# Kernel tuning notes

Hardware: AMD Instinct MI355X
Metric: run time of the kernel (lower is better)

The kernel has to match this reference:

```python
import jax, jax.numpy as jnp
import numpy as np

B, H, HKV, S, D = 1, 32, 4, 2048, 128
NEG = -1e9  # causal mask fill (float32-safe, like torch finfo.min in spirit)


def setup_inputs() -> dict:
    key = jax.random.key(0)
    kq, kk, kv, ks = jax.random.split(key, 4)
    query = jax.random.normal(kq, (B, H, S, D), dtype=jnp.float32)
    k = jax.random.normal(kk, (B, HKV, S, D), dtype=jnp.float32)
    v = jax.random.normal(kv, (B, HKV, S, D), dtype=jnp.float32)
    sinks = jax.random.normal(ks, (H,), dtype=jnp.float32)
    # causal additive mask [B, 1, S, S]
    causal = jnp.where(jnp.tril(jnp.ones((S, S), dtype=bool)), 0.0, NEG).astype(jnp.float32)
    attention_mask = jnp.broadcast_to(causal[None, None], (B, 1, S, S))
    return {"query": query, "key": k, "value": v,
            "attention_mask": attention_mask, "sinks": sinks}


def reference(query, key, value, attention_mask, sinks):
    scaling = 1.0 / jnp.sqrt(jnp.asarray(D, dtype=query.dtype))
    groups = H // HKV
    # repeat_kv: [B, HKV, S, D] -> [B, H, S, D]
    k = jnp.repeat(key, groups, axis=1)
    v = jnp.repeat(value, groups, axis=1)
    # scores [B, H, S, S]
    attn = jnp.einsum('bhqd,bhkd->bhqk', query, k) * scaling
    attn = attn + attention_mask[:, :, :, :attn.shape[-1]]
    # append per-head sink column -> [B, H, S, S+1]
    sink_col = jnp.broadcast_to(sinks.reshape(1, H, 1, 1), (B, H, S, 1)).astype(attn.dtype)
    combined = jnp.concatenate([attn, sink_col], axis=-1)
    combined = combined - jnp.max(combined, axis=-1, keepdims=True)
    probs = jax.nn.softmax(combined, axis=-1)[..., :-1]
    # PV matmul, then [B, H, S, D] -> [B, S, H, D]
    out = jnp.einsum('bhqk,bhkd->bhqd', probs, v)
    return jnp.transpose(out, (0, 2, 1, 3))
```

## Files before the change

kernel.cpp:

```cpp
#include <hip/hip_runtime.h>
#include <hip/hip_bf16.h>

#define NH   32
#define SEQ  2048
#define HD   128
#define KVB  32
#define TILE_ELEMS (KVB * HD)
#define TILE_BYTES 8192

typedef __attribute__((ext_vector_type(8))) short bf16x8;
typedef __attribute__((ext_vector_type(4))) float f32x4;
typedef __attribute__((ext_vector_type(2))) unsigned int u32x2;

#define VMCNT0 asm volatile("s_waitcnt vmcnt(0)" ::: "memory")

static __device__ __forceinline__ unsigned short f2bf(float f) {
  __hip_bfloat16 h = __float2bfloat16(f);
  union { __hip_bfloat16 h; unsigned short u; } c; c.h = h;
  return c.u;
}

__device__ __forceinline__ int swzK(int row, int colByte) {
  return row * 256 + (colByte ^ ((row & 7) << 4));
}
__device__ __forceinline__ int swzV32(int d, int kvByte) {
  return d * 64 + (kvByte ^ ((d & 3) << 4));
}
__device__ __forceinline__ int swzP32(int row, int colByte) {
  return row * 64 + (colByte ^ ((row & 3) << 4));
}

__global__ __launch_bounds__(256)
void convert_kv(const float* __restrict__ K, const float* __restrict__ V,
                char* __restrict__ Ki, char* __restrict__ Vi)
{
  const int b = blockIdx.x;
  const float* Ks = K + (size_t)b * TILE_ELEMS;
  const float* Vs = V + (size_t)b * TILE_ELEMS;
  char* kt = Ki + (size_t)b * TILE_BYTES;
  char* vt = Vi + (size_t)b * TILE_BYTES;
  const int tid  = threadIdx.x;
  const int srow = tid >> 4;
  const int scol = (tid & 15) * 8;
  #pragma unroll
  for (int i = 0; i < 2; ++i) {
    const int row = i * 16 + srow;
    float tk[8], tv[8];
    *(f32x4*)(tk)     = *(const f32x4*)(Ks + row * HD + scol);
    *(f32x4*)(tk + 4) = *(const f32x4*)(Ks + row * HD + scol + 4);
    *(f32x4*)(tv)     = *(const f32x4*)(Vs + row * HD + scol);
    *(f32x4*)(tv + 4) = *(const f32x4*)(Vs + row * HD + scol + 4);
    bf16x8 k8;
    #pragma unroll
    for (int j = 0; j < 8; ++j) k8[j] = (short)f2bf(tk[j]);
    *(bf16x8*)(kt + swzK(row, scol * 2)) = k8;
    #pragma unroll
    for (int j = 0; j < 8; ++j)
      *(unsigned short*)(vt + swzV32(scol + j, row * 2)) = f2bf(tv[j]);
  }
}

__device__ __forceinline__ void stage_tile(const char* kimg, const char* vimg,
                                           char* kb, char* vb, int tid) {
  #pragma unroll
  for (int k = 0; k < 2; ++k)
    __builtin_amdgcn_global_load_lds((const unsigned int*)(kimg + k * 4096 + tid * 16),
                                     (unsigned int*)(kb + k * 4096 + tid * 16), 16, 0, 0);
  #pragma unroll
  for (int k = 0; k < 2; ++k)
    __builtin_amdgcn_global_load_lds((const unsigned int*)(vimg + k * 4096 + tid * 16),
                                     (unsigned int*)(vb + k * 4096 + tid * 16), 16, 0, 0);
}

__global__ __launch_bounds__(256, 4)
void attn_fwd(const float* __restrict__ Q, const float* __restrict__ sinks,
              const char* __restrict__ Ki, const char* __restrict__ Vi,
              float* __restrict__ out)
{
  __shared__ __align__(16) char Kl[2][TILE_BYTES];
  __shared__ __align__(16) char Vl[2][TILE_BYTES];
  __shared__ __align__(16) char Pl[4][1024];

  const int tid  = threadIdx.x;
  const int lane = tid & 63;
  const int w    = tid >> 6;
  const int lr   = lane & 15;
  const int lg   = lane >> 4;

  const int bid = blockIdx.x;
  const int s   = bid >> 8;
  const int a   = bid & 255;
  const int h   = a & 31;
  const int r8  = a >> 5;
  int qt;
  if      (s == 0) qt = 31 - r8;
  else if (s == 1) qt = r8;
  else if (s == 2) qt = 23 - r8;
  else             qt = 8 + r8;
  const int q0  = qt * 64;
  const int nt  = (qt + 1) * 2;
  const int kvh = h >> 3;

  const char* Kt = Ki + (size_t)(kvh * 64) * TILE_BYTES;
  const char* Vt = Vi + (size_t)(kvh * 64) * TILE_BYTES;

  stage_tile(Kt, Vt, Kl[0], Vl[0], tid);

  const float QSC = 0.08838834764831845f * 1.4426950408889634f;
  const float EC  = 17.312340490667562f;

  const int qb   = q0 + w * 16;
  const int qmax = qb + 15;
  const int qme  = qb + lr;

  bf16x8 qa[4];
  {
    const float* qp = Q + (size_t)(h * SEQ + qme) * HD + lg * 8;
    #pragma unroll
    for (int ks = 0; ks < 4; ++ks) {
      float t0[8];
      *(f32x4*)(t0)     = *(const f32x4*)(qp + ks * 32);
      *(f32x4*)(t0 + 4) = *(const f32x4*)(qp + ks * 32 + 4);
      bf16x8 qv;
      #pragma unroll
      for (int jj = 0; jj < 8; ++jj) qv[jj] = (short)f2bf(t0[jj] * QSC);
      qa[ks] = qv;
    }
  }

  f32x4 acc[8];
  f32x4 accl = (f32x4){0.f, 0.f, 0.f, 0.f};
  #pragma unroll
  for (int i = 0; i < 8; ++i) acc[i] = (f32x4){0.f, 0.f, 0.f, 0.f};
  bf16x8 ones;
  #pragma unroll
  for (int i = 0; i < 8; ++i) ones[i] = (short)0x3F80;
  char* pw = Pl[w];

  for (int i = 0; i < nt; ++i) {
    VMCNT0;
    __syncthreads();
    if (i + 1 < nt)
      stage_tile(Kt + (size_t)(i + 1) * TILE_BYTES,
                 Vt + (size_t)(i + 1) * TILE_BYTES,
                 Kl[(i + 1) & 1], Vl[(i + 1) & 1], tid);

    const int kv0 = i * KVB;
    if (kv0 > qmax) continue;
    const char* kb = Kl[i & 1];
    const char* vb = Vl[i & 1];

    f32x4 sc[2];
    __builtin_amdgcn_s_setprio(1);
    #pragma unroll
    for (int cb = 0; cb < 2; ++cb) {
      f32x4 a2 = (f32x4){0.f, 0.f, 0.f, 0.f};
      #pragma unroll
      for (int ks = 0; ks < 4; ++ks) {
        bf16x8 kf = *(const bf16x8*)(kb + swzK(cb * 16 + lr, (ks * 32 + lg * 8) * 2));
        a2 = __builtin_amdgcn_mfma_f32_16x16x32_bf16(kf, qa[ks], a2, 0, 0, 0);
      }
      sc[cb] = a2;
    }
    __builtin_amdgcn_s_setprio(0);

    #pragma unroll
    for (int cb = 0; cb < 2; ++cb) {
      float p[4];
      #pragma unroll
      for (int r = 0; r < 4; ++r) {
        const int kv = kv0 + cb * 16 + lg * 4 + r;
        float e = __builtin_amdgcn_exp2f(sc[cb][r] - EC);
        p[r] = (kv > qme) ? 0.f : e;
      }
      u32x2 wd;
      wd[0] = (unsigned int)f2bf(p[0]) | ((unsigned int)f2bf(p[1]) << 16);
      wd[1] = (unsigned int)f2bf(p[2]) | ((unsigned int)f2bf(p[3]) << 16);
      *(u32x2*)(pw + swzP32(lr, cb * 32 + lg * 8)) = wd;
    }

    bf16x8 pa = *(const bf16x8*)(pw + swzP32(lr, lg * 16));

    accl = __builtin_amdgcn_mfma_f32_16x16x32_bf16(pa, ones, accl, 0, 0, 0);
    __builtin_amdgcn_s_setprio(1);
    #pragma unroll
    for (int ncb = 0; ncb < 8; ++ncb) {
      bf16x8 vf = *(const bf16x8*)(vb + swzV32(ncb * 16 + lr, lg * 16));
      acc[ncb] = __builtin_amdgcn_mfma_f32_16x16x32_bf16(pa, vf, acc[ncb], 0, 0, 0);
    }
    __builtin_amdgcn_s_setprio(0);
  }

  const float sk = sinks[h];
  const float sadd = __builtin_amdgcn_exp2f(sk * 1.4426950408889634f - EC);
  #pragma unroll
  for (int r = 0; r < 4; ++r) {
    const float rd = 1.0f / (accl[r] + sadd);
    const size_t q = qb + lg * 4 + r;
    float* op = out + (q * NH + h) * HD + lr;
    #pragma unroll
    for (int ncb = 0; ncb < 8; ++ncb)
      op[ncb * 16] = acc[ncb][r] * rd;
  }
}

extern "C" void kernel_launch(void* const* d_in, const int* in_sizes, int n_in,
                              void* d_out, int out_size, void* d_ws, size_t ws_size,
                              hipStream_t stream) {
  const float* Q     = (const float*)d_in[0];
  const float* K     = (const float*)d_in[1];
  const float* V     = (const float*)d_in[2];
  const float* sinks = (const float*)d_in[4];
  float* out = (float*)d_out;

  char* Ki = (char*)d_ws;
  char* Vi = Ki + (size_t)256 * TILE_BYTES;

  convert_kv<<<dim3(256), 256, 0, stream>>>(K, V, Ki, Vi);
  attn_fwd<<<dim3(1024), 256, 0, stream>>>(Q, sinks, Ki, Vi, out);
}
```

Measured before the change: 82.84 us.

## Pair causal q-tiles per block, triple-buffer KV, and use fragment-order tile layout

Each block now processes two query tiles (j and 31-j) in sequence, so every block does the same amount of work, and the grid shrinks to 512 blocks. The KV staging ring goes from two to three LDS buffers with a prefetch distance of two, and waits only on the older loads (vmcnt(4)) instead of draining all loads each iteration. The preconverted K/V images are rewritten in MFMA fragment order, so each lane's LDS read becomes a plain lane*16 offset with no XOR swizzle. The cost is more LDS per block and launch bounds reduced to two blocks per SIMD, which lowers occupancy.

```diff
diff --git a/kernel.cpp b/kernel.cpp
--- a/kernel.cpp
+++ b/kernel.cpp
@@ -12,6 +12,7 @@
 typedef __attribute__((ext_vector_type(4))) float f32x4;
 typedef __attribute__((ext_vector_type(2))) unsigned int u32x2;
 
+#define VMCNT4 asm volatile("s_waitcnt vmcnt(4)" ::: "memory")
 #define VMCNT0 asm volatile("s_waitcnt vmcnt(0)" ::: "memory")
 
 static __device__ __forceinline__ unsigned short f2bf(float f) {
@@ -20,12 +21,6 @@
   return c.u;
 }
 
-__device__ __forceinline__ int swzK(int row, int colByte) {
-  return row * 256 + (colByte ^ ((row & 7) << 4));
-}
-__device__ __forceinline__ int swzV32(int d, int kvByte) {
-  return d * 64 + (kvByte ^ ((d & 3) << 4));
-}
 __device__ __forceinline__ int swzP32(int row, int colByte) {
   return row * 64 + (colByte ^ ((row & 3) << 4));
 }
@@ -42,6 +37,8 @@
   const int tid  = threadIdx.x;
   const int srow = tid >> 4;
   const int scol = (tid & 15) * 8;
+  const int ks   = scol >> 5;
+  const int lgk  = (scol >> 3) & 3;
   #pragma unroll
   for (int i = 0; i < 2; ++i) {
     const int row = i * 16 + srow;
@@ -53,10 +50,13 @@
     bf16x8 k8;
     #pragma unroll
     for (int j = 0; j < 8; ++j) k8[j] = (short)f2bf(tk[j]);
-    *(bf16x8*)(kt + swzK(row, scol * 2)) = k8;
-    #pragma unroll
-    for (int j = 0; j < 8; ++j)
-      *(unsigned short*)(vt + swzV32(scol + j, row * 2)) = f2bf(tv[j]);
+    *(bf16x8*)(kt + ((row >> 4) * 4 + ks) * 1024 + (lgk * 16 + (row & 15)) * 16) = k8;
+    #pragma unroll
+    for (int j = 0; j < 8; ++j) {
+      const int d = scol + j;
+      *(unsigned short*)(vt + (d >> 4) * 1024 + ((row >> 3) * 16 + (d & 15)) * 16
+                            + (row & 7) * 2) = f2bf(tv[j]);
+    }
   }
 }
 
@@ -72,13 +72,13 @@
                                      (unsigned int*)(vb + k * 4096 + tid * 16), 16, 0, 0);
 }
 
-__global__ __launch_bounds__(256, 4)
+__global__ __launch_bounds__(256, 2)
 void attn_fwd(const float* __restrict__ Q, const float* __restrict__ sinks,
               const char* __restrict__ Ki, const char* __restrict__ Vi,
               float* __restrict__ out)
 {
-  __shared__ __align__(16) char Kl[2][TILE_BYTES];
-  __shared__ __align__(16) char Vl[2][TILE_BYTES];
+  __shared__ __align__(16) char Kl[3][TILE_BYTES];
+  __shared__ __align__(16) char Vl[3][TILE_BYTES];
   __shared__ __align__(16) char Pl[4][1024];
 
   const int tid  = threadIdx.x;
@@ -88,119 +88,129 @@
   const int lg   = lane >> 4;
 
   const int bid = blockIdx.x;
-  const int s   = bid >> 8;
-  const int a   = bid & 255;
-  const int h   = a & 31;
-  const int r8  = a >> 5;
-  int qt;
-  if      (s == 0) qt = 31 - r8;
-  else if (s == 1) qt = r8;
-  else if (s == 2) qt = 23 - r8;
-  else             qt = 8 + r8;
-  const int q0  = qt * 64;
-  const int nt  = (qt + 1) * 2;
+  const int h   = bid >> 4;
+  const int j   = bid & 15;
   const int kvh = h >> 3;
+  const int nt0 = 2 * (32 - j);
+  const int nt1 = 2 * (j + 1);
+  const int ntot = nt0 + nt1;
 
   const char* Kt = Ki + (size_t)(kvh * 64) * TILE_BYTES;
   const char* Vt = Vi + (size_t)(kvh * 64) * TILE_BYTES;
 
   stage_tile(Kt, Vt, Kl[0], Vl[0], tid);
+  stage_tile(Kt + TILE_BYTES, Vt + TILE_BYTES, Kl[1], Vl[1], tid);
 
   const float QSC = 0.08838834764831845f * 1.4426950408889634f;
   const float EC  = 17.312340490667562f;
 
-  const int qb   = q0 + w * 16;
-  const int qmax = qb + 15;
-  const int qme  = qb + lr;
-
-  bf16x8 qa[4];
-  {
-    const float* qp = Q + (size_t)(h * SEQ + qme) * HD + lg * 8;
-    #pragma unroll
-    for (int ks = 0; ks < 4; ++ks) {
-      float t0[8];
-      *(f32x4*)(t0)     = *(const f32x4*)(qp + ks * 32);
-      *(f32x4*)(t0 + 4) = *(const f32x4*)(qp + ks * 32 + 4);
-      bf16x8 qv;
-      #pragma unroll
-      for (int jj = 0; jj < 8; ++jj) qv[jj] = (short)f2bf(t0[jj] * QSC);
-      qa[ks] = qv;
-    }
-  }
-
-  f32x4 acc[8];
-  f32x4 accl = (f32x4){0.f, 0.f, 0.f, 0.f};
-  #pragma unroll
-  for (int i = 0; i < 8; ++i) acc[i] = (f32x4){0.f, 0.f, 0.f, 0.f};
   bf16x8 ones;
   #pragma unroll
   for (int i = 0; i < 8; ++i) ones[i] = (short)0x3F80;
   char* pw = Pl[w];
-
-  for (int i = 0; i < nt; ++i) {
-    VMCNT0;
-    __syncthreads();
-    if (i + 1 < nt)
-      stage_tile(Kt + (size_t)(i + 1) * TILE_BYTES,
-                 Vt + (size_t)(i + 1) * TILE_BYTES,
-                 Kl[(i + 1) & 1], Vl[(i + 1) & 1], tid);
-
-    const int kv0 = i * KVB;
-    if (kv0 > qmax) continue;
-    const char* kb = Kl[i & 1];
-    const char* vb = Vl[i & 1];
-
-    f32x4 sc[2];
-    __builtin_amdgcn_s_setprio(1);
-    #pragma unroll
-    for (int cb = 0; cb < 2; ++cb) {
-      f32x4 a2 = (f32x4){0.f, 0.f, 0.f, 0.f};
+  const char* pl16 = (const char*)0 + lane * 16;
+
+  int g = 0;
+  #pragma unroll 1
+  for (int su = 0; su < 2; ++su) {
+    const int qt = su ? j : (31 - j);
+    const int q0 = qt * 64;
+    const int nt = su ? nt1 : nt0;
+    const int qb   = q0 + w * 16;
+    const int qmax = qb + 15;
+    const int qme  = qb + lr;
+
+    bf16x8 qa[4];
+    {
+      const float* qp = Q + (size_t)(h * SEQ + qme) * HD + lg * 8;
       #pragma unroll
       for (int ks = 0; ks < 4; ++ks) {
-        bf16x8 kf = *(const bf16x8*)(kb + swzK(cb * 16 + lr, (ks * 32 + lg * 8) * 2));
-        a2 = __builtin_amdgcn_mfma_f32_16x16x32_bf16(kf, qa[ks], a2, 0, 0, 0);
-      }
-      sc[cb] = a2;
-    }
-    __builtin_amdgcn_s_setprio(0);
-
-    #pragma unroll
-    for (int cb = 0; cb < 2; ++cb) {
-      float p[4];
-      #pragma unroll
-      for (int r = 0; r < 4; ++r) {
-        const int kv = kv0 + cb * 16 + lg * 4 + r;
-        float e = __builtin_amdgcn_exp2f(sc[cb][r] - EC);
-        p[r] = (kv > qme) ? 0.f : e;
-      }
-      u32x2 wd;
-      wd[0] = (unsigned int)f2bf(p[0]) | ((unsigned int)f2bf(p[1]) << 16);
-      wd[1] = (unsigned int)f2bf(p[2]) | ((unsigned int)f2bf(p[3]) << 16);
-      *(u32x2*)(pw + swzP32(lr, cb * 32 + lg * 8)) = wd;
-    }
-
-    bf16x8 pa = *(const bf16x8*)(pw + swzP32(lr, lg * 16));
-
-    accl = __builtin_amdgcn_mfma_f32_16x16x32_bf16(pa, ones, accl, 0, 0, 0);
-    __builtin_amdgcn_s_setprio(1);
-    #pragma unroll
-    for (int ncb = 0; ncb < 8; ++ncb) {
-      bf16x8 vf = *(const bf16x8*)(vb + swzV32(ncb * 16 + lr, lg * 16));
-      acc[ncb] = __builtin_amdgcn_mfma_f32_16x16x32_bf16(pa, vf, acc[ncb], 0, 0, 0);
-    }
-    __builtin_amdgcn_s_setprio(0);
-  }
-
-  const float sk = sinks[h];
-  const float sadd = __builtin_amdgcn_exp2f(sk * 1.4426950408889634f - EC);
-  #pragma unroll
-  for (int r = 0; r < 4; ++r) {
-    const float rd = 1.0f / (accl[r] + sadd);
-    const size_t q = qb + lg * 4 + r;
-    float* op = out + (q * NH + h) * HD + lr;
-    #pragma unroll
-    for (int ncb = 0; ncb < 8; ++ncb)
-      op[ncb * 16] = acc[ncb][r] * rd;
+        float t0[8];
+        *(f32x4*)(t0)     = *(const f32x4*)(qp + ks * 32);
+        *(f32x4*)(t0 + 4) = *(const f32x4*)(qp + ks * 32 + 4);
+        bf16x8 qv;
+        #pragma unroll
+        for (int jj = 0; jj < 8; ++jj) qv[jj] = (short)f2bf(t0[jj] * QSC);
+        qa[ks] = qv;
+      }
+    }
+
+    f32x4 acc[8];
+    f32x4 accl = (f32x4){0.f, 0.f, 0.f, 0.f};
+    #pragma unroll
+    for (int i = 0; i < 8; ++i) acc[i] = (f32x4){0.f, 0.f, 0.f, 0.f};
+
+    for (int i = 0; i < nt; ++i, ++g) {
+      if (g == ntot - 1) { VMCNT0; } else { VMCNT4; }
+      __builtin_amdgcn_s_barrier();
+
+      const int gn = g + 2;
+      if (gn < ntot) {
+        const int src = (gn < nt0) ? gn : (gn - nt0);
+        const int bb  = gn % 3;
+        stage_tile(Kt + (size_t)src * TILE_BYTES, Vt + (size_t)src * TILE_BYTES,
+                   Kl[bb], Vl[bb], tid);
+      }
+
+      const int kv0 = i * KVB;
+      if (kv0 > qmax) continue;
+      const char* kb = Kl[g % 3] + lane * 16;
+      const char* vb = Vl[g % 3] + lane * 16;
+
+      f32x4 sc[2];
+      __builtin_amdgcn_s_setprio(1);
+      #pragma unroll
+      for (int cb = 0; cb < 2; ++cb) {
+        f32x4 a2 = (f32x4){0.f, 0.f, 0.f, 0.f};
+        #pragma unroll
+        for (int ks = 0; ks < 4; ++ks) {
+          bf16x8 kf = *(const bf16x8*)(kb + (cb * 4 + ks) * 1024);
+          a2 = __builtin_amdgcn_mfma_f32_16x16x32_bf16(kf, qa[ks], a2, 0, 0, 0);
+        }
+        sc[cb] = a2;
+      }
+      __builtin_amdgcn_s_setprio(0);
+
+      float lsum0 = 0.f;
+      #pragma unroll
+      for (int cb = 0; cb < 2; ++cb) {
+        float p[4];
+        #pragma unroll
+        for (int r = 0; r < 4; ++r) {
+          const int kv = kv0 + cb * 16 + lg * 4 + r;
+          float e = __builtin_amdgcn_exp2f(sc[cb][r] - EC);
+          p[r] = (kv > qme) ? 0.f : e;
+        }
+        u32x2 wd;
+        wd[0] = (unsigned int)f2bf(p[0]) | ((unsigned int)f2bf(p[1]) << 16);
+        wd[1] = (unsigned int)f2bf(p[2]) | ((unsigned int)f2bf(p[3]) << 16);
+        *(u32x2*)(pw + swzP32(lr, cb * 32 + lg * 8)) = wd;
+      }
+      (void)lsum0;
+
+      bf16x8 pa = *(const bf16x8*)(pw + swzP32(lr, lg * 16));
+
+      accl = __builtin_amdgcn_mfma_f32_16x16x32_bf16(pa, ones, accl, 0, 0, 0);
+      __builtin_amdgcn_s_setprio(1);
+      #pragma unroll
+      for (int ncb = 0; ncb < 8; ++ncb) {
+        bf16x8 vf = *(const bf16x8*)(vb + ncb * 1024);
+        acc[ncb] = __builtin_amdgcn_mfma_f32_16x16x32_bf16(pa, vf, acc[ncb], 0, 0, 0);
+      }
+      __builtin_amdgcn_s_setprio(0);
+    }
+
+    const float sk = sinks[h];
+    const float sadd = __builtin_amdgcn_exp2f(sk * 1.4426950408889634f - EC);
+    #pragma unroll
+    for (int r = 0; r < 4; ++r) {
+      const float rd = 1.0f / (accl[r] + sadd);
+      const size_t q = qb + lg * 4 + r;
+      float* op = out + (q * NH + h) * HD + lr;
+      #pragma unroll
+      for (int ncb = 0; ncb < 8; ++ncb)
+        op[ncb * 16] = acc[ncb][r] * rd;
+    }
   }
 }
 
@@ -217,5 +227,5 @@
   char* Vi = Ki + (size_t)256 * TILE_BYTES;
 
   convert_kv<<<dim3(256), 256, 0, stream>>>(K, V, Ki, Vi);
-  attn_fwd<<<dim3(1024), 256, 0, stream>>>(Q, sinks, Ki, Vi, out);
-}
+  attn_fwd<<<dim3(512), 256, 0, stream>>>(Q, sinks, Ki, Vi, out);
+}
```

Result: slower. 84.51 us (+2.0%).
